# Kernel tuning notes

Hardware: AMD Instinct MI355X
Metric: run time of the kernel (lower is better)

Reference implementation:

```python
import jax, jax.numpy as jnp
from jax import lax
import numpy as np

B = 131072   # batch
M = 16       # in_channel (message dim, m=2^k with k=4)
NCH = 8      # n_channel (complex symbols)
CD = 16      # 2*n_channel
TAPS = 3     # rayleigh channel taps
R = 0.5      # code rate k/n
EBNO = 10.0 ** (7.0 / 10.0)
EPS = 1e-5


def setup_inputs() -> dict:
    ks = jax.random.split(jax.random.key(0), 48)
    f32 = jnp.float32
    def lin(i, o, n):
        return jax.random.normal(ks[i], (o, n), f32) / np.float32(np.sqrt(n))
    def cw(i, o, c, k):
        return jax.random.normal(ks[i], (o, c, k), f32) / np.float32(np.sqrt(c * k))
    def bv(i, n):
        return 0.01 * jax.random.normal(ks[i], (n,), f32)
    return dict(
        x=jax.random.normal(ks[0], (B, M), f32),
        noise=jax.random.normal(ks[1], (B, CD), f32) / np.float32(np.sqrt(2 * R * EBNO)),
        fading=jax.random.normal(ks[2], (B, TAPS, 2), f32),
        ew1=lin(3, M, M), eb1=bv(4, M),
        ew2=lin(5, CD, M), eb2=bv(6, CD),
        ec1w=cw(7, NCH, 1, 2), ec1b=bv(8, NCH),
        ec2w=cw(9, NCH, NCH, 4), ec2b=bv(10, NCH),
        ec3w=cw(11, NCH, NCH, 2), ec3b=bv(12, NCH),
        ec4w=cw(13, NCH, NCH, 2), ec4b=bv(14, NCH),
        ew3=lin(15, CD, 2 * CD), eb3=bv(16, CD),
        bng=jnp.ones((CD,), f32), bnb=jnp.zeros((CD,), f32),
        pw1=lin(17, 2 * CD, CD), pb1=bv(18, 2 * CD),
        pw2=lin(19, 4 * CD, 2 * CD), pb2=bv(20, 4 * CD),
        pw3=lin(21, CD // 2, 4 * CD), pb3=bv(22, CD // 2),
        pw4=lin(23, 2, CD // 2), pb4=bv(24, 2),
        dw1=lin(25, CD, CD), db1=bv(26, CD),
        dc1w=cw(27, NCH, 1, 2), dc1b=bv(28, NCH),
        dc2w=cw(29, NCH, NCH, 4), dc2b=bv(30, NCH),
        dc3w=cw(31, NCH, NCH, 2), dc3b=bv(32, NCH),
        dc4w=cw(33, NCH, NCH, 2), dc4b=bv(34, NCH),
        dw2=lin(35, CD, 2 * CD), db2=bv(36, CD),
        dw3=lin(37, CD, CD), db3=bv(38, CD),
        dw4=lin(39, M, CD), db4=bv(40, M),
    )


def _conv(h, w, bias, s):
    y = lax.conv_general_dilated(h, w, (s,), 'VALID', dimension_numbers=('NCH', 'OIH', 'NCH'))
    return y + bias[None, :, None]


def reference(x, noise, fading, ew1, eb1, ew2, eb2, ec1w, ec1b, ec2w, ec2b, ec3w, ec3b,
              ec4w, ec4b, ew3, eb3, bng, bnb, pw1, pb1, pw2, pb2, pw3, pb3, pw4, pb4,
              dw1, db1, dc1w, dc1b, dc2w, dc2b, dc3w, dc3b, dc4w, dc4b, dw2, db2,
              dw3, db3, dw4, db4):
    elu, tanh = jax.nn.elu, jnp.tanh
    Bn = x.shape[0]
    # ---- encoder ----
    h = elu(x @ ew1.T + eb1)
    h = elu(h @ ew2.T + eb2)                       # (B, CD)
    h = h[:, None, :]                              # (B, 1, CD)
    h = tanh(_conv(h, ec1w, ec1b, 1))              # (B, NCH, 15)
    h = tanh(_conv(h, ec2w, ec2b, 2))              # (B, NCH, 6)
    h = tanh(_conv(h, ec3w, ec3b, 1))              # (B, NCH, 5)
    h = tanh(_conv(h, ec4w, ec4b, 1))              # (B, NCH, 4)
    h = h.reshape(Bn, 2 * bng.shape[0])            # (B, 2*CD)
    h = h @ ew3.T + eb3                            # (B, CD)
    mu = h.mean(0)
    var = h.var(0)                                 # biased var (torch BN training mode)
    enc = (h - mu) / jnp.sqrt(var + EPS) * bng + bnb
    # ---- rayleigh multipath channel: vectorized complex FIR over taps ----
    taps = fading.shape[1]
    xc = enc.reshape(Bn, -1, 2)                    # (B, NCH, 2) re/im pairs
    n_sym = xc.shape[1]
    pad = taps - 1
    padded = jnp.pad(xc, ((0, 0), (pad, pad), (0, 0)))
    idx = jnp.arange(n_sym + taps - 1)[:, None] + jnp.arange(taps)[None, :]
    win = padded[:, idx]                           # (B, L_out, taps, 2)
    ff = fading[:, ::-1]                           # per-example flipped taps
    yr = jnp.einsum('blt,bt->bl', win[..., 0], ff[..., 0]) - jnp.einsum('blt,bt->bl', win[..., 1], ff[..., 1])
    yi = jnp.einsum('blt,bt->bl', win[..., 0], ff[..., 1]) + jnp.einsum('blt,bt->bl', win[..., 1], ff[..., 0])
    y = jnp.stack([yr, yi], -1)[:, :n_sym]         # drop trailing taps-1 samples
    c = y.reshape(Bn, 2 * n_sym) + noise
    # ---- channel parameter estimation ----
    p = elu(c @ pw1.T + pb1)
    p = tanh(p @ pw2.T + pb2)
    p = tanh(p @ pw3.T + pb3)
    hp = p @ pw4.T + pb4                           # (B, 2) estimated complex h
    # ---- transform: complex division x / h ----
    cc = c.reshape(Bn, n_sym, 2)
    hr, hi = hp[:, 0:1], hp[:, 1:2]
    den = hr * hr + hi * hi
    tr = (cc[..., 0] * hr + cc[..., 1] * hi) / den
    ti = (cc[..., 1] * hr - cc[..., 0] * hi) / den
    t = jnp.stack([tr, ti], -1).reshape(Bn, 2 * n_sym)
    # ---- decoder ----
    d = tanh(t @ dw1.T + db1)
    d = d[:, None, :]
    d = tanh(_conv(d, dc1w, dc1b, 1))
    d = tanh(_conv(d, dc2w, dc2b, 2))
    d = tanh(_conv(d, dc3w, dc3b, 1))
    d = tanh(_conv(d, dc4w, dc4b, 1))
    d = d.reshape(Bn, -1)
    d = tanh(d @ dw2.T + db2)
    d = tanh(d @ dw3.T + db3)
    return d @ dw4.T + db4
```

## Files before the change

### kernel.cpp

```cpp
#include <hip/hip_runtime.h>


#define BTOT 131072
#define NT2  65536
#define BLK  128
#define NBLK 512
#define NW   6768

typedef float v2 __attribute__((ext_vector_type(2)));

constexpr int EW1 = 0;     constexpr int EB1 = 256;
constexpr int EW2 = 272;   constexpr int EB2 = 528;
constexpr int EC1W = 544;  constexpr int EC1B = 560;
constexpr int EC2W = 568;  constexpr int EC2B = 824;
constexpr int EC3W = 832;  constexpr int EC3B = 960;
constexpr int EC4W = 968;  constexpr int EC4B = 1096;
constexpr int EW3 = 1104;  constexpr int EB3 = 1616;
constexpr int BNG = 1632;  constexpr int BNB = 1648;
constexpr int PW1 = 1664;  constexpr int PB1 = 2176;
constexpr int PW2 = 2208;  constexpr int PB2 = 4256;
constexpr int PW3 = 4320;  constexpr int PB3 = 4832;
constexpr int PW4 = 4840;  constexpr int PB4 = 4856;
constexpr int DW1 = 4864;  constexpr int DB1 = 5120;
constexpr int DC1W = 5136; constexpr int DC1B = 5152;
constexpr int DC2W = 5160; constexpr int DC2B = 5416;
constexpr int DC3W = 5424; constexpr int DC3B = 5552;
constexpr int DC4W = 5560; constexpr int DC4B = 5688;
constexpr int DW2 = 5696;  constexpr int DB2 = 6208;
constexpr int DW3 = 6224;  constexpr int DB3 = 6480;
constexpr int DW4 = 6496;  constexpr int DB4 = 6752;

constexpr size_t WS_W    = 0;
constexpr size_t WS_PART = 32768;

__device__ __forceinline__ v2 sp(float s) { v2 r; r.x = s; r.y = s; return r; }
__device__ __forceinline__ float bf2f(unsigned int u) {
  union { unsigned int i; float f; } v; v.i = u << 16; return v.f;
}
__device__ __forceinline__ unsigned short f2bf(float f) {
  union { float f; unsigned int i; } v; v.f = f;
  unsigned int x = v.i;
  return (unsigned short)((x + 0x7fffu + ((x >> 16) & 1u)) >> 16);
}
__device__ __forceinline__ void unpack8(uint4 u, float* f) {
  f[0] = bf2f(u.x & 0xffffu); f[1] = bf2f(u.x >> 16);
  f[2] = bf2f(u.y & 0xffffu); f[3] = bf2f(u.y >> 16);
  f[4] = bf2f(u.z & 0xffffu); f[5] = bf2f(u.z >> 16);
  f[6] = bf2f(u.w & 0xffffu); f[7] = bf2f(u.w >> 16);
}
__device__ __forceinline__ int sniff_bf16(const void* bng) {
  return *(const unsigned int*)bng != 0x3F800000u;
}
__device__ __forceinline__ void load16(const void* base, int b, int isbf, float* f) {
  if (isbf) {
    const uint4* p = (const uint4*)((const unsigned short*)base + (size_t)b * 16);
    unpack8(p[0], f); unpack8(p[1], f + 8);
  } else {
    const float4* p = (const float4*)((const float*)base + (size_t)b * 16);
#pragma unroll
    for (int q = 0; q < 4; q++) {
      float4 v = p[q];
      f[4 * q] = v.x; f[4 * q + 1] = v.y; f[4 * q + 2] = v.z; f[4 * q + 3] = v.w;
    }
  }
}
__device__ __forceinline__ void load16_2(const void* base, int bA, int bB, int isbf,
                                         v2* f) {
  float a[16], b[16];
  load16(base, bA, isbf, a);
  load16(base, bB, isbf, b);
#pragma unroll
  for (int j = 0; j < 16; j++) { f[j].x = a[j]; f[j].y = b[j]; }
}
__device__ __forceinline__ void store16(void* base, int b, int isbf, const float* f) {
  if (isbf) {
    unsigned int ov[8];
#pragma unroll
    for (int j = 0; j < 8; j++)
      ov[j] = (unsigned int)f2bf(f[2 * j]) | ((unsigned int)f2bf(f[2 * j + 1]) << 16);
    uint4* op = (uint4*)((unsigned short*)base + (size_t)b * 16);
    op[0] = make_uint4(ov[0], ov[1], ov[2], ov[3]);
    op[1] = make_uint4(ov[4], ov[5], ov[6], ov[7]);
  } else {
    float4* op = (float4*)((float*)base + (size_t)b * 16);
#pragma unroll
    for (int q = 0; q < 4; q++)
      op[q] = make_float4(f[4 * q], f[4 * q + 1], f[4 * q + 2], f[4 * q + 3]);
  }
}
__device__ __forceinline__ float tanh_f(float x) {
  float e = __expf(2.0f * x);
  return 1.0f - 2.0f * __builtin_amdgcn_rcpf(e + 1.0f);
}
__device__ __forceinline__ v2 tanh_v(v2 x) {
  v2 r; r.x = tanh_f(x.x); r.y = tanh_f(x.y); return r;
}
__device__ __forceinline__ v2 elu_v(v2 x) {
  v2 r;
  r.x = x.x > 0.0f ? x.x : __expf(x.x) - 1.0f;
  r.y = x.y > 0.0f ? x.y : __expf(x.y) - 1.0f;
  return r;
}

template <int OUT, int IN, int WOFF, int BOFF, int ACT>
__device__ __forceinline__ void dense2(const float* w, const v2* in, v2* out) {
#pragma unroll
  for (int m = 0; m < OUT; m++) {
    v2 v = sp(w[BOFF + m]);
#pragma unroll
    for (int k = 0; k < IN; k += 4) {
      float4 wv = *(const float4*)(w + WOFF + m * IN + k);
      v += in[k] * wv.x; v += in[k + 1] * wv.y;
      v += in[k + 2] * wv.z; v += in[k + 3] * wv.w;
    }
    if (ACT == 1) v = elu_v(v);
    if (ACT == 2) v = tanh_v(v);
    out[m] = v;
  }
}

template <int W1, int B1, int W2, int B2, int W3, int B3, int W4, int B4>
__device__ __forceinline__ void conv_chain2(const float* w, const v2 h[16],
                                            v2 flat[32]) {
  v2 c1[4][8];
  v2 c2[6][8];
#pragma unroll
  for (int p = 0; p < 6; p++) {
    const int p0 = (p == 0) ? 0 : (2 * p + 2);
#pragma unroll
    for (int pos = p0; pos <= 2 * p + 3; ++pos) {
#pragma unroll
      for (int o = 0; o < 8; o++) {
        float2 wv = *(const float2*)(w + W1 + o * 2);
        v2 v = h[pos] * wv.x + h[pos + 1] * wv.y + sp(w[B1 + o]);
        c1[pos & 3][o] = tanh_v(v);
      }
    }
#pragma unroll
    for (int o = 0; o < 8; o++) {
      v2 v = sp(w[B2 + o]);
#pragma unroll
      for (int i = 0; i < 8; i++) {
        float4 wv = *(const float4*)(w + W2 + (o * 8 + i) * 4);
        v += c1[(2 * p) & 3][i] * wv.x;
        v += c1[(2 * p + 1) & 3][i] * wv.y;
        v += c1[(2 * p + 2) & 3][i] * wv.z;
        v += c1[(2 * p + 3) & 3][i] * wv.w;
      }
      c2[p][o] = tanh_v(v);
    }
  }
  v2 c3[5][8];
#pragma unroll
  for (int p = 0; p < 5; p++) {
#pragma unroll
    for (int o = 0; o < 8; o++) {
      v2 v = sp(w[B3 + o]);
#pragma unroll
      for (int i = 0; i < 8; i++) {
        float2 wv = *(const float2*)(w + W3 + (o * 8 + i) * 2);
        v += c2[p][i] * wv.x + c2[p + 1][i] * wv.y;
      }
      c3[p][o] = tanh_v(v);
    }
  }
#pragma unroll
  for (int p = 0; p < 4; p++) {
#pragma unroll
    for (int o = 0; o < 8; o++) {
      v2 v = sp(w[B4 + o]);
#pragma unroll
      for (int i = 0; i < 8; i++) {
        float2 wv = *(const float2*)(w + W4 + (o * 8 + i) * 2);
        v += c3[p][i] * wv.x + c3[p + 1][i] * wv.y;
      }
      flat[o * 4 + p] = tanh_v(v);
    }
  }
}

struct Segs {
  const void* src[40];
  int cnt[40];
  int off[40];
};

__global__ __launch_bounds__(256) void k_convert(Segs s, const void* __restrict__ bng_src,
                                                 float* __restrict__ dst) {
  const int isbf = sniff_bf16(bng_src);
  const int seg = blockIdx.x;
  const int n = s.cnt[seg];
  const int o = s.off[seg];
  if (isbf) {
    const unsigned short* p = (const unsigned short*)s.src[seg];
    for (int i = threadIdx.x; i < n; i += 256) dst[o + i] = bf2f((unsigned int)p[i]);
  } else {
    const float* p = (const float*)s.src[seg];
    for (int i = threadIdx.x; i < n; i += 256) dst[o + i] = p[i];
  }
}

__global__ __launch_bounds__(BLK, 1) void k_enc(const void* __restrict__ x,
                                                const void* __restrict__ bng_src,
                                                const float* __restrict__ wg,
                                                float* __restrict__ partials,
                                                void* __restrict__ outbuf) {
  const int isbf = sniff_bf16(bng_src);
  const int t = blockIdx.x * BLK + threadIdx.x;
  const int bA = t, bB = t + NT2;

  v2 xv[16];
  load16_2(x, bA, bB, isbf, xv);

  __shared__ float sw[NW];
  for (int i = threadIdx.x; i < NW / 4; i += BLK)
    ((float4*)sw)[i] = ((const float4*)wg)[i];
  __syncthreads();

  v2 he[16];
  {
    v2 h1[16], h2[16];
    dense2<16, 16, EW1, EB1, 1>(sw, xv, h1);
    dense2<16, 16, EW2, EB2, 1>(sw, h1, h2);
    v2 flat[32];
    conv_chain2<EC1W, EC1B, EC2W, EC2B, EC3W, EC3B, EC4W, EC4B>(sw, h2, flat);
    dense2<16, 32, EW3, EB3, 0>(sw, flat, he);
  }

  {
    float a[16], b[16];
#pragma unroll
    for (int j = 0; j < 16; j++) { a[j] = he[j].x; b[j] = he[j].y; }
    store16(outbuf, bA, isbf, a);
    store16(outbuf, bB, isbf, b);
  }

  __shared__ float part[2][32];
  const int lane = threadIdx.x & 63;
  const int wid = threadIdx.x >> 6;
#pragma unroll
  for (int j = 0; j < 16; j++) {
    float s = he[j].x + he[j].y;
    float q = he[j].x * he[j].x + he[j].y * he[j].y;
#pragma unroll
    for (int m = 32; m >= 1; m >>= 1) {
      s += __shfl_xor(s, m, 64);
      q += __shfl_xor(q, m, 64);
    }
    if (lane == 0) { part[wid][j] = s; part[wid][16 + j] = q; }
  }
  __syncthreads();
  if (threadIdx.x < 32)
    partials[blockIdx.x * 32 + threadIdx.x] = part[0][threadIdx.x] + part[1][threadIdx.x];
}

__global__ __launch_bounds__(BLK, 1) void k_main(const void* __restrict__ noise,
                                                 const void* __restrict__ fading,
                                                 const void* __restrict__ bng_src,
                                                 const float* __restrict__ wbuf,
                                                 const float* __restrict__ partials,
                                                 void* __restrict__ out) {
  const int isbf = sniff_bf16(bng_src);
  const int t = blockIdx.x * BLK + threadIdx.x;
  const int bA = t, bB = t + NT2;

  v2 enc[16];
  load16_2(out, bA, bB, isbf, enc);
  v2 nz[16];
  load16_2(noise, bA, bB, isbf, nz);
  v2 fr[3], fi[3];
  if (isbf) {
    const unsigned int* fa =
        (const unsigned int*)((const unsigned short*)fading + (size_t)bA * 6);
    const unsigned int* fb =
        (const unsigned int*)((const unsigned short*)fading + (size_t)bB * 6);
#pragma unroll
    for (int j = 0; j < 3; j++) {
      unsigned int ua = fa[j], ub = fb[j];
      fr[j].x = bf2f(ua & 0xffffu); fi[j].x = bf2f(ua >> 16);
      fr[j].y = bf2f(ub & 0xffffu); fi[j].y = bf2f(ub >> 16);
    }
  } else {
    const float2* fa = (const float2*)((const float*)fading + (size_t)bA * 6);
    const float2* fb = (const float2*)((const float*)fading + (size_t)bB * 6);
#pragma unroll
    for (int j = 0; j < 3; j++) {
      float2 a = fa[j], b = fb[j];
      fr[j].x = a.x; fi[j].x = a.y;
      fr[j].y = b.x; fi[j].y = b.y;
    }
  }

  __shared__ float sw[NW];
  for (int i = threadIdx.x; i < NW / 4; i += BLK)
    ((float4*)sw)[i] = ((const float4*)wbuf)[i];

  __shared__ float redf[BLK][4];
  __shared__ float tot[32];
  __shared__ float scsh[32];
  {
    const float4* p4 = (const float4*)partials;
    float a0x = 0, a0y = 0, a0z = 0, a0w = 0;
    float a1x = 0, a1y = 0, a1z = 0, a1w = 0;
    float a2x = 0, a2y = 0, a2z = 0, a2w = 0;
    float a3x = 0, a3y = 0, a3z = 0, a3w = 0;
#pragma unroll 1
    for (int m = 0; m < 32; m += 4) {
      float4 q0 = p4[threadIdx.x + (m + 0) * BLK];
      float4 q1 = p4[threadIdx.x + (m + 1) * BLK];
      float4 q2 = p4[threadIdx.x + (m + 2) * BLK];
      float4 q3 = p4[threadIdx.x + (m + 3) * BLK];
      a0x += q0.x; a0y += q0.y; a0z += q0.z; a0w += q0.w;
      a1x += q1.x; a1y += q1.y; a1z += q1.z; a1w += q1.w;
      a2x += q2.x; a2y += q2.y; a2z += q2.z; a2w += q2.w;
      a3x += q3.x; a3y += q3.y; a3z += q3.z; a3w += q3.w;
    }
    redf[threadIdx.x][0] = a0x + a1x + a2x + a3x;
    redf[threadIdx.x][1] = a0y + a1y + a2y + a3y;
    redf[threadIdx.x][2] = a0z + a1z + a2z + a3z;
    redf[threadIdx.x][3] = a0w + a1w + a2w + a3w;
  }
  __syncthreads();
  if (threadIdx.x < 32) {
    const int ch = threadIdx.x;
    const int j = ch >> 2, comp = ch & 3;
    float v = 0.0f;
#pragma unroll
    for (int k = 0; k < 16; k++) v += redf[j + k * 8][comp];
    tot[ch] = v;
  }
  __syncthreads();
  if (threadIdx.x < 16) {
    const float invB = 1.0f / (float)BTOT;
    float mu = tot[threadIdx.x] * invB;
    float var = tot[16 + threadIdx.x] * invB - mu * mu;
    float rstd = rsqrtf(var + 1e-5f);
    float sc = sw[BNG + threadIdx.x] * rstd;
    scsh[threadIdx.x] = sc;
    scsh[16 + threadIdx.x] = sw[BNB + threadIdx.x] - mu * sc;
  }
  __syncthreads();

#pragma unroll
  for (int j = 0; j < 16; j++) enc[j] = enc[j] * scsh[j] + sp(scsh[16 + j]);

  v2 c[16];
#pragma unroll
  for (int l = 0; l < 8; l++) {
    v2 ar = sp(0.0f), ai = sp(0.0f);
#pragma unroll
    for (int j = 0; j < 3; j++) {
      if (l - j >= 0) {
        v2 xr = enc[2 * (l - j)], xi = enc[2 * (l - j) + 1];
        ar += xr * fr[j] - xi * fi[j];
        ai += xr * fi[j] + xi * fr[j];
      }
    }
    c[2 * l] = ar + nz[2 * l];
    c[2 * l + 1] = ai + nz[2 * l + 1];
  }
  v2 p1[32];
  dense2<32, 16, PW1, PB1, 1>(sw, c, p1);
  v2 p3[8];
#pragma unroll
  for (int j = 0; j < 8; j++) p3[j] = sp(sw[PB3 + j]);
#pragma unroll
  for (int n0 = 0; n0 < 64; n0 += 4) {
    v2 tv[4];
#pragma unroll
    for (int u = 0; u < 4; u++) {
      const int n = n0 + u;
      v2 v = sp(sw[PB2 + n]);
#pragma unroll
      for (int k = 0; k < 32; k += 4) {
        float4 wv = *(const float4*)(sw + PW2 + n * 32 + k);
        v += p1[k] * wv.x; v += p1[k + 1] * wv.y;
        v += p1[k + 2] * wv.z; v += p1[k + 3] * wv.w;
      }
      tv[u] = tanh_v(v);
    }
#pragma unroll
    for (int j = 0; j < 8; j++) {
      float4 wv = *(const float4*)(sw + PW3 + j * 64 + n0);
      p3[j] += tv[0] * wv.x + tv[1] * wv.y + tv[2] * wv.z + tv[3] * wv.w;
    }
  }
#pragma unroll
  for (int j = 0; j < 8; j++) p3[j] = tanh_v(p3[j]);
  v2 hr = sp(sw[PB4 + 0]), hi = sp(sw[PB4 + 1]);
#pragma unroll
  for (int k = 0; k < 8; k++) {
    hr += p3[k] * sw[PW4 + k];
    hi += p3[k] * sw[PW4 + 8 + k];
  }
  v2 den = hr * hr + hi * hi;
  v2 inv; inv.x = __builtin_amdgcn_rcpf(den.x); inv.y = __builtin_amdgcn_rcpf(den.y);
  v2 tt[16];
#pragma unroll
  for (int l = 0; l < 8; l++) {
    v2 c0 = c[2 * l], c1v = c[2 * l + 1];
    tt[2 * l] = (c0 * hr + c1v * hi) * inv;
    tt[2 * l + 1] = (c1v * hr - c0 * hi) * inv;
  }
  v2 d1[16];
  dense2<16, 16, DW1, DB1, 2>(sw, tt, d1);
  v2 flat[32];
  conv_chain2<DC1W, DC1B, DC2W, DC2B, DC3W, DC3B, DC4W, DC4B>(sw, d1, flat);
  v2 d2[16], d3[16], o[16];
  dense2<16, 32, DW2, DB2, 2>(sw, flat, d2);
  dense2<16, 16, DW3, DB3, 2>(sw, d2, d3);
  dense2<16, 16, DW4, DB4, 0>(sw, d3, o);

  {
    float a[16], b[16];
#pragma unroll
    for (int j = 0; j < 16; j++) { a[j] = o[j].x; b[j] = o[j].y; }
    store16(out, bA, isbf, a);
    store16(out, bB, isbf, b);
  }
}

extern "C" void kernel_launch(void* const* d_in, const int* in_sizes, int n_in,
                              void* d_out, int out_size, void* d_ws, size_t ws_size,
                              hipStream_t stream) {
  float* wbuf = (float*)((char*)d_ws + WS_W);
  float* partials = (float*)((char*)d_ws + WS_PART);

  static const int offs[40] = {
      EW1, EB1, EW2, EB2, EC1W, EC1B, EC2W, EC2B, EC3W, EC3B, EC4W, EC4B,
      EW3, EB3, BNG, BNB, PW1, PB1, PW2, PB2, PW3, PB3, PW4, PB4,
      DW1, DB1, DC1W, DC1B, DC2W, DC2B, DC3W, DC3B, DC4W, DC4B,
      DW2, DB2, DW3, DB3, DW4, DB4};
  Segs segs;
  for (int k = 0; k < 40; k++) {
    segs.src[k] = d_in[3 + k];
    segs.cnt[k] = in_sizes[3 + k];
    segs.off[k] = offs[k];
  }
  const void* bng_src = d_in[17];

  k_convert<<<40, 256, 0, stream>>>(segs, bng_src, wbuf);
  k_enc<<<NBLK, BLK, 0, stream>>>(d_in[0], bng_src, wbuf, partials, d_out);
  k_main<<<NBLK, BLK, 0, stream>>>(d_in[1], d_in[2], bng_src, wbuf, partials, d_out);
}
```

Baseline: 254.7 us.

## Fuse encoder and main kernels with a grid-wide atomic barrier for batch-norm stats

Merges the encoder and main kernels into one launch. A software grid barrier (an atomic counter reset by the convert kernel) waits for all blocks' batch-norm partials before normalization. Encoder outputs stay in registers instead of being written to and reread from global memory, which also removes one launch and the shared-memory weight reload. The barrier needs all 512 blocks to be co-resident, which holds on this GPU with one block per CU-slot, but it adds spin-wait cost and a deadlock risk if residency fails.

```diff
diff --git a/kernel.cpp b/kernel.cpp
--- a/kernel.cpp
+++ b/kernel.cpp
@@ -31,6 +31,7 @@
 constexpr int DW4 = 6496;  constexpr int DB4 = 6752;
 
 constexpr size_t WS_W    = 0;
+constexpr size_t WS_BAR  = 28672;
 constexpr size_t WS_PART = 32768;
 
 __device__ __forceinline__ v2 sp(float s) { v2 r; r.x = s; r.y = s; return r; }
@@ -186,7 +187,9 @@
 };
 
 __global__ __launch_bounds__(256) void k_convert(Segs s, const void* __restrict__ bng_src,
-                                                 float* __restrict__ dst) {
+                                                 float* __restrict__ dst,
+                                                 unsigned int* __restrict__ bar) {
+  if (blockIdx.x == 0 && threadIdx.x == 0) *bar = 0u;
   const int isbf = sniff_bf16(bng_src);
   const int seg = blockIdx.x;
   const int n = s.cnt[seg];
@@ -200,11 +203,14 @@
   }
 }
 
-__global__ __launch_bounds__(BLK, 1) void k_enc(const void* __restrict__ x,
-                                                const void* __restrict__ bng_src,
-                                                const float* __restrict__ wg,
-                                                float* __restrict__ partials,
-                                                void* __restrict__ outbuf) {
+__global__ __launch_bounds__(BLK, 1) void k_fused(const void* __restrict__ x,
+                                                  const void* __restrict__ noise,
+                                                  const void* __restrict__ fading,
+                                                  const void* __restrict__ bng_src,
+                                                  const float* __restrict__ wg,
+                                                  float* __restrict__ partials,
+                                                  unsigned int* __restrict__ bar,
+                                                  void* __restrict__ out) {
   const int isbf = sniff_bf16(bng_src);
   const int t = blockIdx.x * BLK + threadIdx.x;
   const int bA = t, bB = t + NT2;
@@ -227,14 +233,6 @@
     dense2<16, 32, EW3, EB3, 0>(sw, flat, he);
   }
 
-  {
-    float a[16], b[16];
-#pragma unroll
-    for (int j = 0; j < 16; j++) { a[j] = he[j].x; b[j] = he[j].y; }
-    store16(outbuf, bA, isbf, a);
-    store16(outbuf, bB, isbf, b);
-  }
-
   __shared__ float part[2][32];
   const int lane = threadIdx.x & 63;
   const int wid = threadIdx.x >> 6;
@@ -249,23 +247,7 @@
     }
     if (lane == 0) { part[wid][j] = s; part[wid][16 + j] = q; }
   }
-  __syncthreads();
-  if (threadIdx.x < 32)
-    partials[blockIdx.x * 32 + threadIdx.x] = part[0][threadIdx.x] + part[1][threadIdx.x];
-}
-
-__global__ __launch_bounds__(BLK, 1) void k_main(const void* __restrict__ noise,
-                                                 const void* __restrict__ fading,
-                                                 const void* __restrict__ bng_src,
-                                                 const float* __restrict__ wbuf,
-                                                 const float* __restrict__ partials,
-                                                 void* __restrict__ out) {
-  const int isbf = sniff_bf16(bng_src);
-  const int t = blockIdx.x * BLK + threadIdx.x;
-  const int bA = t, bB = t + NT2;
-
-  v2 enc[16];
-  load16_2(out, bA, bB, isbf, enc);
+
   v2 nz[16];
   load16_2(noise, bA, bB, isbf, nz);
   v2 fr[3], fi[3];
@@ -291,9 +273,19 @@
     }
   }
 
-  __shared__ float sw[NW];
-  for (int i = threadIdx.x; i < NW / 4; i += BLK)
-    ((float4*)sw)[i] = ((const float4*)wbuf)[i];
+  __syncthreads();
+  if (threadIdx.x < 32)
+    partials[blockIdx.x * 32 + threadIdx.x] = part[0][threadIdx.x] + part[1][threadIdx.x];
+
+  if (threadIdx.x == 0) {
+    __threadfence();
+    __hip_atomic_fetch_add(bar, 1u, __ATOMIC_RELAXED, __HIP_MEMORY_SCOPE_AGENT);
+    while (__hip_atomic_load(bar, __ATOMIC_RELAXED, __HIP_MEMORY_SCOPE_AGENT) <
+           (unsigned int)NBLK)
+      __builtin_amdgcn_s_sleep(2);
+    __threadfence();
+  }
+  __syncthreads();
 
   __shared__ float redf[BLK][4];
   __shared__ float tot[32];
@@ -342,7 +334,7 @@
   __syncthreads();
 
 #pragma unroll
-  for (int j = 0; j < 16; j++) enc[j] = enc[j] * scsh[j] + sp(scsh[16 + j]);
+  for (int j = 0; j < 16; j++) he[j] = he[j] * scsh[j] + sp(scsh[16 + j]);
 
   v2 c[16];
 #pragma unroll
@@ -351,7 +343,7 @@
 #pragma unroll
     for (int j = 0; j < 3; j++) {
       if (l - j >= 0) {
-        v2 xr = enc[2 * (l - j)], xi = enc[2 * (l - j) + 1];
+        v2 xr = he[2 * (l - j)], xi = he[2 * (l - j) + 1];
         ar += xr * fr[j] - xi * fi[j];
         ai += xr * fi[j] + xi * fr[j];
       }
@@ -425,6 +417,7 @@
                               hipStream_t stream) {
   float* wbuf = (float*)((char*)d_ws + WS_W);
   float* partials = (float*)((char*)d_ws + WS_PART);
+  unsigned int* bar = (unsigned int*)((char*)d_ws + WS_BAR);
 
   static const int offs[40] = {
       EW1, EB1, EW2, EB2, EC1W, EC1B, EC2W, EC2B, EC3W, EC3B, EC4W, EC4B,
@@ -439,7 +432,7 @@
   }
   const void* bng_src = d_in[17];
 
-  k_convert<<<40, 256, 0, stream>>>(segs, bng_src, wbuf);
-  k_enc<<<NBLK, BLK, 0, stream>>>(d_in[0], bng_src, wbuf, partials, d_out);
-  k_main<<<NBLK, BLK, 0, stream>>>(d_in[1], d_in[2], bng_src, wbuf, partials, d_out);
-}
+  k_convert<<<40, 256, 0, stream>>>(segs, bng_src, wbuf, bar);
+  k_fused<<<NBLK, BLK, 0, stream>>>(d_in[0], d_in[1], d_in[2], bng_src, wbuf,
+                                    partials, bar, d_out);
+}
```

Result: slower. 405.3 us (+59.1%).
